# Optimization experiments

Measured on AMD Instinct MI355X. Metric: run time of the kernel, lower is better.

## Reference

```python
import jax, jax.numpy as jnp
import numpy as np

HIDDEN = 2048
INTER = 4096
HEADS = 32
HEAD_DIM = INTER // HEADS  # 128
STATE = 128
GROUPS = 1
CONV_K = 4
CHUNK = 256
EPS = 1e-5
CONV_DIM = INTER + 2 * GROUPS * STATE  # 4352
DT_MIN, DT_MAX = 0.0, 100.0
BATCH, SEQ = 2, 4096


def _segment_sum(x):
    """Stable segment sum: returns (..., T, T) with entry [i,j] = sum_{k=j+1..i} x[k] (-inf above diag)."""
    T = x.shape[-1]
    xx = jnp.broadcast_to(x[..., None], x.shape + (T,))
    mask_lower = jnp.tril(jnp.ones((T, T), bool), -1)
    xx = jnp.where(mask_lower, xx, 0.0)
    seg = jnp.cumsum(xx, axis=-2)
    mask_incl = jnp.tril(jnp.ones((T, T), bool), 0)
    return jnp.where(mask_incl, seg, -jnp.inf)


def setup_inputs() -> dict:
    key = jax.random.key(0)
    ks = jax.random.split(key, 8)
    std = 0.02
    return {
        "hidden_states": jax.random.normal(ks[0], (BATCH, SEQ, HIDDEN), jnp.float32),
        "in_proj_w": jax.random.normal(ks[1], (INTER + CONV_DIM + HEADS, HIDDEN), jnp.float32) * std,
        "conv_w": jax.random.normal(ks[2], (CONV_DIM, 1, CONV_K), jnp.float32) * std,
        "conv_b": jnp.zeros((CONV_DIM,), jnp.float32),
        "A_log": jnp.log(jax.random.uniform(ks[3], (HEADS,), jnp.float32, 1.0, 16.0)),
        "dt_bias": jax.random.normal(ks[4], (HEADS,), jnp.float32) * 0.1,
        "D": jnp.ones((HEADS,), jnp.float32),
        "norm_w": jnp.ones((INTER,), jnp.float32),
        "out_proj_w": jax.random.normal(ks[5], (HIDDEN, INTER), jnp.float32) * (std / np.sqrt(48.0)),
    }


def reference(hidden_states, in_proj_w, conv_w, conv_b, A_log, dt_bias, D, norm_w, out_proj_w):
    b, s, _ = hidden_states.shape
    # in_proj and split into gate / conv-input / dt
    proj = hidden_states @ in_proj_w.T
    gate, hBC, dt = jnp.split(proj, [INTER, INTER + CONV_DIM], axis=-1)

    # causal depthwise conv1d (padding k-1 left, truncate to seq_len) + SiLU
    x = jnp.transpose(hBC, (0, 2, 1))  # (b, conv_dim, s)
    x = jax.lax.conv_general_dilated(
        x, conv_w, window_strides=(1,), padding=[(CONV_K - 1, 0)],
        dimension_numbers=("NCH", "OIH", "NCH"), feature_group_count=CONV_DIM)
    x = x + conv_b[None, :, None]
    hBC = jax.nn.silu(jnp.transpose(x, (0, 2, 1)))  # (b, s, conv_dim)

    xs, B, C = jnp.split(hBC, [INTER, INTER + GROUPS * STATE], axis=-1)

    A = -jnp.exp(A_log)  # (h,)
    dt = jnp.clip(jax.nn.softplus(dt + dt_bias), DT_MIN, DT_MAX)  # (b, s, h)

    xs = xs.reshape(b, s, HEADS, HEAD_DIM)
    rep = HEADS // GROUPS
    Bm = jnp.repeat(B.reshape(b, s, GROUPS, STATE), rep, axis=2)  # (b,s,h,n)
    Cm = jnp.repeat(C.reshape(b, s, GROUPS, STATE), rep, axis=2)

    pad = (-s) % CHUNK

    def padseq(t):
        return jnp.pad(t, ((0, 0), (0, pad)) + ((0, 0),) * (t.ndim - 2))

    D_res = D[None, None, :, None] * padseq(xs)  # (b, S, h, p)
    xdt = padseq(xs * dt[..., None])
    Ad = padseq(A[None, None, :] * dt)  # (b, S, h)
    Bm, Cm = padseq(Bm), padseq(Cm)

    nc = (s + pad) // CHUNK
    xdt = xdt.reshape(b, nc, CHUNK, HEADS, HEAD_DIM)
    Ad = jnp.transpose(Ad.reshape(b, nc, CHUNK, HEADS), (0, 3, 1, 2))  # (b,h,c,l)
    Bm = Bm.reshape(b, nc, CHUNK, HEADS, STATE)
    Cm = Cm.reshape(b, nc, CHUNK, HEADS, STATE)

    A_cum = jnp.cumsum(Ad, axis=-1)  # (b,h,c,l)

    # 1) intra-chunk (diagonal block) output
    L = jnp.exp(_segment_sum(Ad))  # (b,h,c,l,l)
    G = jnp.einsum("bclhn,bcshn->bclsh", Cm, Bm)
    M = G * jnp.transpose(L, (0, 2, 3, 4, 1))
    Y_diag = jnp.einsum("bclsh,bcshp->bclhp", M, xdt)

    # 2) per-chunk final states
    decay_states = jnp.exp(A_cum[:, :, :, -1:] - A_cum)  # (b,h,c,l)
    B_decay = Bm * jnp.transpose(decay_states, (0, 2, 3, 1))[..., None]
    states = jnp.einsum("bclhn,bclhp->bchpn", B_decay, xdt)  # (b,c,h,p,n)

    # 3) inter-chunk recurrence
    states = jnp.concatenate([jnp.zeros_like(states[:, :1]), states], axis=1)  # (b,c+1,h,p,n)
    chunk_sums = jnp.pad(A_cum[:, :, :, -1], ((0, 0), (0, 0), (1, 0)))  # (b,h,c+1)
    decay_chunk = jnp.exp(_segment_sum(chunk_sums))  # (b,h,c+1,c+1)
    decay_chunk = jnp.transpose(decay_chunk, (0, 2, 3, 1))  # (b,c,z,h)
    new_states = jnp.einsum("bczh,bchpn->bzhpn", decay_chunk, states)
    states = new_states[:, :-1]  # (b,c,h,p,n) state entering each chunk

    # 4) state -> output contribution
    state_decay = jnp.exp(A_cum)  # (b,h,c,l)
    Y_off = jnp.einsum("bclhn,bchpn->bclhp", Cm, states) * jnp.transpose(state_decay, (0, 2, 3, 1))[..., None]

    y = (Y_diag + Y_off).reshape(b, nc * CHUNK, HEADS, HEAD_DIM) + D_res
    y = y[:, :s].reshape(b, s, INTER)

    # gated RMSNorm
    y = y * jax.nn.silu(gate)
    var = jnp.mean(y * y, axis=-1, keepdims=True)
    y = y * jax.lax.rsqrt(var + EPS) * norm_w

    return y @ out_proj_w.T
```

## Files before the change

kernel.cpp:

```cpp
#include <hip/hip_runtime.h>

#define SEQ     4096
#define BATCH   2
#define NROWS   8192
#define HID     2048
#define INTER_  4096
#define NHEADS  32
#define HDIM    128
#define NSTATE  128
#define CDIM    4352
#define NPROJ_  8480
#define NPAD    8704
#define NCH     16
#define CHUNK_  256

typedef __attribute__((ext_vector_type(8))) short bf16x8;
typedef __attribute__((ext_vector_type(4))) short short4v;
typedef __attribute__((ext_vector_type(4))) float f32x4;

#define AS1 __attribute__((address_space(1)))
#define AS3 __attribute__((address_space(3)))

__device__ __forceinline__ float bf2f(short s) {
  union { unsigned u; float f; } x;
  x.u = ((unsigned)(unsigned short)s) << 16;
  return x.f;
}
__device__ __forceinline__ short f2bf(float f) {
  union { float f; unsigned u; } x; x.f = f;
  unsigned r = x.u + 0x7FFFu + ((x.u >> 16) & 1u);
  return (short)(r >> 16);
}

__global__ void cvt_bf16(const float* __restrict__ in, short* __restrict__ out,
                         int n4, int nsrc4) {
  int i = blockIdx.x * 256 + threadIdx.x;
  if (i >= n4) return;
  short4v o = {0, 0, 0, 0};
  if (i < nsrc4) {
    f32x4 v = *(const f32x4*)(in + (size_t)i * 4);
    o = (short4v){ f2bf(v.x), f2bf(v.y), f2bf(v.z), f2bf(v.w) };
  }
  *(short4v*)(out + (size_t)i * 4) = o;
}

template<int MODE>
__global__ __launch_bounds__(512, 1)
void gemm256(const short* __restrict__ A, const short* __restrict__ Bw,
             int M, int N, int K, int nM,
             float* __restrict__ outF, short* __restrict__ gate,
             short* __restrict__ hbc, float* __restrict__ dtraw)
{
  __shared__ __align__(16) short lds[2][2][2][256 * 32];
  const int tid = threadIdx.x;
  const int lane = tid & 63, wave = tid >> 6;
  const int l16 = lane & 15, lhi = lane >> 4;
  const int wm = wave >> 2, wn = wave & 3;

  const int bm = blockIdx.x % nM, bn = blockIdx.x / nM;
  const size_t row0 = (size_t)bm * 256;
  const int    col0 = bn * 256;

  const short* Ab  = A + row0 * K;
  const short* Bbp = Bw + (size_t)col0 * K;

  f32x4 acc[8][4];
  #pragma unroll
  for (int m = 0; m < 8; ++m)
    #pragma unroll
    for (int n = 0; n < 4; ++n) acc[m][n] = (f32x4){0.f, 0.f, 0.f, 0.f};

  auto stage = [&](int bufq, int mat, int kh, int ko) {
    const short* gsrc = mat ? Bbp : Ab;
    short* base = &lds[bufq][mat][kh][0];
    #pragma unroll
    for (int j = 0; j < 2; ++j) {
      int u = j * 512 + tid;
      int r = u >> 2;
      int g = (u & 3) ^ ((r >> 1) & 3);
      __builtin_amdgcn_global_load_lds(
          (const AS1 unsigned*)(gsrc + (size_t)r * K + ko + kh * 32 + g * 8),
          (AS3 unsigned*)(base + (j * 512 + wave * 64) * 8), 16, 0, 0);
    }
  };
  auto readA = [&](int bufq, int kh, int mh, bf16x8* a) {
    const short* base = &lds[bufq][0][kh][0];
    #pragma unroll
    for (int f = 0; f < 4; ++f) {
      int rr = wm * 128 + mh * 64 + f * 16 + l16;
      int g = lhi ^ ((rr >> 1) & 3);
      a[f] = *(const bf16x8*)(base + rr * 32 + g * 8);
    }
  };
  auto readB = [&](int bufq, int kh, bf16x8* b) {
    const short* base = &lds[bufq][1][kh][0];
    #pragma unroll
    for (int f = 0; f < 4; ++f) {
      int rr = wn * 64 + f * 16 + l16;
      int g = lhi ^ ((rr >> 1) & 3);
      b[f] = *(const bf16x8*)(base + rr * 32 + g * 8);
    }
  };

  const int nt = K / 64;
  stage(0, 0, 0, 0); stage(0, 1, 0, 0); stage(0, 0, 1, 0); stage(0, 1, 1, 0);
  asm volatile("s_waitcnt vmcnt(4)" ::: "memory");
  __builtin_amdgcn_s_barrier();

  for (int t = 0; t < nt; ++t) {
    const int buf = t & 1, nb = buf ^ 1;
    const int kon = (t + 1) * 64;
    const bool pf = (t + 1 < nt);

    #pragma unroll
    for (int kh = 0; kh < 2; ++kh) {
      if (pf) { stage(nb, 0, kh, kon); stage(nb, 1, kh, kon); }
      bf16x8 a[8], b[4];
      readA(buf, kh, 0, a); readA(buf, kh, 1, a + 4); readB(buf, kh, b);
      __builtin_amdgcn_s_setprio(1);
      #pragma unroll
      for (int mf = 0; mf < 8; ++mf)
        #pragma unroll
        for (int nf = 0; nf < 4; ++nf)
          acc[mf][nf] = __builtin_amdgcn_mfma_f32_16x16x32_bf16(a[mf], b[nf], acc[mf][nf], 0, 0, 0);
      __builtin_amdgcn_s_setprio(0);
      if (pf || kh == 0) {
        if (pf) asm volatile("s_waitcnt vmcnt(4)" ::: "memory");
        else    asm volatile("s_waitcnt vmcnt(0)" ::: "memory");
        __builtin_amdgcn_s_barrier();
      }
    }
  }

  #pragma unroll
  for (int mh = 0; mh < 2; ++mh) {
    #pragma unroll
    for (int f = 0; f < 4; ++f) {
      #pragma unroll
      for (int nf = 0; nf < 4; ++nf) {
        #pragma unroll
        for (int j = 0; j < 4; ++j) {
          int gr = (int)row0 + wm * 128 + mh * 64 + f * 16 + lhi * 4 + j;
          int gc = col0 + wn * 64 + nf * 16 + l16;
          float v = acc[mh * 4 + f][nf][j];
          if (MODE == 0) {
            outF[(size_t)gr * N + gc] = v;
          } else {
            if (gc < INTER_)             gate[(size_t)gr * INTER_ + gc] = f2bf(v);
            else if (gc < INTER_ + CDIM) hbc[(size_t)gr * CDIM + (gc - INTER_)] = f2bf(v);
            else if (gc < NPROJ_)        dtraw[(size_t)gr * NHEADS + (gc - INTER_ - CDIM)] = v;
          }
        }
      }
    }
  }
}

__global__ __launch_bounds__(256)
void conv_t(const short* __restrict__ hbc, const float* __restrict__ cw,
            const float* __restrict__ cb, short* __restrict__ xsT,
            short* __restrict__ Bb, short* __restrict__ Cb, short* __restrict__ BbT)
{
  __shared__ short sOut[64][130];
  int ct = blockIdx.y;
  int cl = threadIdx.x & 127;
  int rh = threadIdx.x >> 7;
  int c = ct * 128 + cl;
  int row0 = blockIdx.x * 64;
  int s0 = row0 & (SEQ - 1);
  float w0 = cw[c * 4 + 0], w1 = cw[c * 4 + 1], w2 = cw[c * 4 + 2], w3 = cw[c * 4 + 3];
  float bias = cb[c];
  int r0 = rh * 32;
  float h0, h1, h2;
  h0 = (s0 + r0 - 3 >= 0) ? bf2f(hbc[(size_t)(row0 + r0 - 3) * CDIM + c]) : 0.f;
  h1 = (s0 + r0 - 2 >= 0) ? bf2f(hbc[(size_t)(row0 + r0 - 2) * CDIM + c]) : 0.f;
  h2 = (s0 + r0 - 1 >= 0) ? bf2f(hbc[(size_t)(row0 + r0 - 1) * CDIM + c]) : 0.f;

  for (int r = r0; r < r0 + 32; ++r) {
    float xin = bf2f(hbc[(size_t)(row0 + r) * CDIM + c]);
    float a = bias + w0 * h0 + w1 * h1 + w2 * h2 + w3 * xin;
    h0 = h1; h1 = h2; h2 = xin;
    float v = a / (1.f + expf(-a));
    short bv = f2bf(v);
    if (ct < 33) sOut[r][cl] = bv;
    if (ct == 32)      Bb[(size_t)(row0 + r) * NSTATE + cl] = bv;
    else if (ct == 33) Cb[(size_t)(row0 + r) * NSTATE + cl] = bv;
  }
  if (ct >= 33) return;
  __syncthreads();
  int p = threadIdx.x >> 1, sh = (threadIdx.x & 1) * 32;
  int b = row0 >> 12;
  size_t dst;
  short* outp;
  if (ct < 32) { outp = xsT; dst = ((size_t)(b * 32 + ct) * 128 + p) * SEQ + s0 + sh; }
  else         { outp = BbT; dst = ((size_t)b * 128 + p) * SEQ + s0 + sh; }
  #pragma unroll
  for (int g = 0; g < 8; ++g) {
    short4v o;
    o[0] = sOut[sh + g * 4 + 0][p];
    o[1] = sOut[sh + g * 4 + 1][p];
    o[2] = sOut[sh + g * 4 + 2][p];
    o[3] = sOut[sh + g * 4 + 3][p];
    *(short4v*)(outp + dst + g * 4) = o;
  }
}

__global__ void dt_proc(const float* __restrict__ dtraw, const float* __restrict__ dtb,
                        float* __restrict__ dtT, int n) {
  int i = blockIdx.x * 256 + threadIdx.x;
  if (i >= n) return;
  float x = dtraw[i] + dtb[i & (NHEADS - 1)];
  float sp = (x > 20.f) ? x : log1pf(expf(x));
  float d = fminf(fmaxf(sp, 0.f), 100.f);
  int row = i >> 5, h = i & 31;
  dtT[(size_t)h * NROWS + row] = d;
}

__global__ __launch_bounds__(256)
void ssm_state(const short* __restrict__ xsT, const short* __restrict__ BbT,
               const float* __restrict__ dtT, const float* __restrict__ Alog,
               short* __restrict__ csb, float* __restrict__ dAsum)
{
  int blk = blockIdx.x;
  int h = blk & 31, cc = (blk >> 5) & 15, b = blk >> 9;
  int tid = threadIdx.x, lane = tid & 63, wave = tid >> 6;
  int l16 = lane & 15, lhi = lane >> 4;
  int s0 = cc * CHUNK_;

  __shared__ float acum[256];
  __shared__ float sdt[256];
  { float Ah = -expf(Alog[h]);
    float d = dtT[(size_t)h * NROWS + (size_t)b * SEQ + s0 + tid];
    sdt[tid] = d; acum[tid] = Ah * d; }
  for (int off = 1; off < 256; off <<= 1) {
    __syncthreads();
    float v = (tid >= off) ? acum[tid - off] : 0.f;
    __syncthreads();
    acum[tid] += v;
  }
  __syncthreads();
  float alast = acum[255];

  const short* xbase = xsT + ((size_t)(b * 32 + h) * 128) * SEQ + s0;
  const short* bbase = BbT + ((size_t)b * 128) * SEQ + s0;

  f32x4 acc[2][8];
  #pragma unroll
  for (int m = 0; m < 2; ++m)
    #pragma unroll
    for (int n = 0; n < 8; ++n) acc[m][n] = (f32x4){0.f, 0.f, 0.f, 0.f};

  for (int lt0 = 0; lt0 < 256; lt0 += 32) {
    float fe[8];
    #pragma unroll
    for (int e = 0; e < 8; ++e) {
      int kl = lt0 + lhi * 8 + e;
      fe[e] = sdt[kl] * __expf(alast - acum[kl]);
    }
    bf16x8 af[2];
    #pragma unroll
    for (int m = 0; m < 2; ++m) {
      bf16x8 raw = *(const bf16x8*)(xbase + (size_t)(wave * 32 + m * 16 + l16) * SEQ + lt0 + lhi * 8);
      bf16x8 sc;
      #pragma unroll
      for (int e = 0; e < 8; ++e) sc[e] = f2bf(bf2f(raw[e]) * fe[e]);
      af[m] = sc;
    }
    #pragma unroll
    for (int n = 0; n < 8; ++n) {
      bf16x8 bfv = *(const bf16x8*)(bbase + (size_t)(n * 16 + l16) * SEQ + lt0 + lhi * 8);
      acc[0][n] = __builtin_amdgcn_mfma_f32_16x16x32_bf16(af[0], bfv, acc[0][n], 0, 0, 0);
      acc[1][n] = __builtin_amdgcn_mfma_f32_16x16x32_bf16(af[1], bfv, acc[1][n], 0, 0, 0);
    }
  }
  size_t base = (size_t)blk * 16384;
  #pragma unroll
  for (int m = 0; m < 2; ++m)
    #pragma unroll
    for (int n = 0; n < 8; ++n)
      #pragma unroll
      for (int j = 0; j < 4; ++j) {
        int p = wave * 32 + m * 16 + lhi * 4 + j;
        int ng = n * 16 + l16;
        csb[base + (size_t)p * NSTATE + ng] = f2bf(acc[m][n][j]);
      }
  if (tid == 0) dAsum[blk] = alast;
}

__global__ void ssm_scan(short* __restrict__ csb, const float* __restrict__ dAsum) {
  int idx = blockIdx.x * 256 + threadIdx.x;
  int np = idx & 16383;
  int bh = idx >> 14;
  int h = bh & 31, b = bh >> 5;
  float run = 0.f;
  #pragma unroll
  for (int c = 0; c < NCH; ++c) {
    size_t base = ((size_t)((b * NCH + c) * NHEADS + h)) * 16384 + np;
    float v = bf2f(csb[base]);
    csb[base] = f2bf(run);
    run = run * __expf(dAsum[(b * NCH + c) * NHEADS + h]) + v;
  }
}

__global__ __launch_bounds__(256)
void ssm_y(const short* __restrict__ xsT, const short* __restrict__ Bb,
           const short* __restrict__ Cb, const float* __restrict__ dtT,
           const float* __restrict__ Alog, const float* __restrict__ Dv,
           const short* __restrict__ csb, short* __restrict__ gateY)
{
  int blk = blockIdx.y, lt = blockIdx.x;
  int h = blk & 31, cc = (blk >> 5) & 15, b = blk >> 9;
  int tid = threadIdx.x, lane = tid & 63, wave = tid >> 6;
  int l16 = lane & 15, lhi = lane >> 4;
  int s0 = cc * CHUNK_;
  size_t row0 = (size_t)b * SEQ + s0;

  __shared__ float acum[256];
  __shared__ float sdt[256];
  __shared__ __align__(16) short M_lds[64 * 264];

  { float Ah = -expf(Alog[h]);
    float d = dtT[(size_t)h * NROWS + row0 + tid];
    sdt[tid] = d; acum[tid] = Ah * d; }
  for (int off = 1; off < 256; off <<= 1) {
    __syncthreads();
    float v = (tid >= off) ? acum[tid - off] : 0.f;
    __syncthreads();
    acum[tid] += v;
  }
  __syncthreads();

  float Dh = Dv[h];

  {
    f32x4 acc1[4][4];
    #pragma unroll
    for (int m = 0; m < 4; ++m)
      #pragma unroll
      for (int n = 0; n < 4; ++n) acc1[m][n] = (f32x4){0.f, 0.f, 0.f, 0.f};
    for (int kk = 0; kk < NSTATE; kk += 32) {
      bf16x8 af[4], bv[4];
      #pragma unroll
      for (int m = 0; m < 4; ++m)
        af[m] = *(const bf16x8*)(Cb + (row0 + lt * 64 + m * 16 + l16) * NSTATE + kk + lhi * 8);
      #pragma unroll
      for (int n = 0; n < 4; ++n)
        bv[n] = *(const bf16x8*)(Bb + (row0 + wave * 64 + n * 16 + l16) * NSTATE + kk + lhi * 8);
      #pragma unroll
      for (int m = 0; m < 4; ++m)
        #pragma unroll
        for (int n = 0; n < 4; ++n)
          acc1[m][n] = __builtin_amdgcn_mfma_f32_16x16x32_bf16(af[m], bv[n], acc1[m][n], 0, 0, 0);
    }
    float as_[4]; int sg_[4];
    #pragma unroll
    for (int n = 0; n < 4; ++n) { sg_[n] = wave * 64 + n * 16 + l16; as_[n] = acum[sg_[n]]; }
    #pragma unroll
    for (int m = 0; m < 4; ++m) {
      #pragma unroll
      for (int j = 0; j < 4; ++j) {
        int ll = m * 16 + lhi * 4 + j;
        int lg = lt * 64 + ll;
        float al = acum[lg];
        float dinv = Dh / fmaxf(sdt[lg], 1e-20f);
        #pragma unroll
        for (int n = 0; n < 4; ++n) {
          float v = 0.f;
          if (sg_[n] <= lg) {
            v = acc1[m][n][j] * __expf(al - as_[n]);
            if (sg_[n] == lg) v += dinv;
          }
          M_lds[ll * 264 + wave * 64 + n * 16 + l16] = f2bf(v);
        }
      }
    }
  }
  __syncthreads();

  const short* xbase = xsT + ((size_t)(b * 32 + h) * 128) * SEQ + s0;

  f32x4 accY[4][2];
  #pragma unroll
  for (int m = 0; m < 4; ++m) { accY[m][0] = (f32x4){0,0,0,0}; accY[m][1] = (f32x4){0,0,0,0}; }
  int smax = (lt + 1) * 64;
  for (int st = 0; st < smax; st += 32) {
    float fe[8];
    #pragma unroll
    for (int e = 0; e < 8; ++e) fe[e] = sdt[st + lhi * 8 + e];
    bf16x8 bv2[2];
    #pragma unroll
    for (int n = 0; n < 2; ++n) {
      bf16x8 raw = *(const bf16x8*)(xbase + (size_t)(wave * 32 + n * 16 + l16) * SEQ + st + lhi * 8);
      bf16x8 sc;
      #pragma unroll
      for (int e = 0; e < 8; ++e) sc[e] = f2bf(bf2f(raw[e]) * fe[e]);
      bv2[n] = sc;
    }
    #pragma unroll
    for (int m = 0; m < 4; ++m) {
      bf16x8 a = *(const bf16x8*)(M_lds + (m * 16 + l16) * 264 + st + lhi * 8);
      accY[m][0] = __builtin_amdgcn_mfma_f32_16x16x32_bf16(a, bv2[0], accY[m][0], 0, 0, 0);
      accY[m][1] = __builtin_amdgcn_mfma_f32_16x16x32_bf16(a, bv2[1], accY[m][1], 0, 0, 0);
    }
  }

  f32x4 accO[4][2];
  #pragma unroll
  for (int m = 0; m < 4; ++m) { accO[m][0] = (f32x4){0,0,0,0}; accO[m][1] = (f32x4){0,0,0,0}; }
  const short* sbase = csb + (size_t)blk * 16384;
  for (int nt = 0; nt < NSTATE; nt += 32) {
    bf16x8 bv2[2];
    #pragma unroll
    for (int n = 0; n < 2; ++n) {
      int p = wave * 32 + n * 16 + l16;
      bv2[n] = *(const bf16x8*)(sbase + (size_t)p * NSTATE + nt + lhi * 8);
    }
    #pragma unroll
    for (int m = 0; m < 4; ++m) {
      bf16x8 a = *(const bf16x8*)(Cb + (row0 + lt * 64 + m * 16 + l16) * NSTATE + nt + lhi * 8);
      accO[m][0] = __builtin_amdgcn_mfma_f32_16x16x32_bf16(a, bv2[0], accO[m][0], 0, 0, 0);
      accO[m][1] = __builtin_amdgcn_mfma_f32_16x16x32_bf16(a, bv2[1], accO[m][1], 0, 0, 0);
    }
  }

  #pragma unroll
  for (int m = 0; m < 4; ++m) {
    #pragma unroll
    for (int j = 0; j < 4; ++j) {
      int ll = m * 16 + lhi * 4 + j;
      float e = __expf(acum[lt * 64 + ll]);
      size_t row = row0 + lt * 64 + ll;
      #pragma unroll
      for (int n = 0; n < 2; ++n) {
        int p = wave * 32 + n * 16 + l16;
        size_t adr = row * INTER_ + h * HDIM + p;
        float yv = accY[m][n][j] + e * accO[m][n][j];
        float g = bf2f(gateY[adr]);
        gateY[adr] = f2bf(yv * g / (1.f + expf(-g)));
      }
    }
  }
}

__global__ __launch_bounds__(256)
void gate_norm(short* __restrict__ ybf, const float* __restrict__ nw)
{
  int row = blockIdx.x;
  int tid = threadIdx.x;
  size_t base = (size_t)row * INTER_;
  float vals[16];
  float ss = 0.f;
  #pragma unroll
  for (int i = 0; i < 16; ++i) {
    int idx = tid + i * 256;
    float v = bf2f(ybf[base + idx]);
    vals[i] = v;
    ss += v * v;
  }
  #pragma unroll
  for (int off = 32; off > 0; off >>= 1) ss += __shfl_down(ss, off);
  __shared__ float ws4[4];
  if ((tid & 63) == 0) ws4[tid >> 6] = ss;
  __syncthreads();
  float tot = ws4[0] + ws4[1] + ws4[2] + ws4[3];
  float scale = rsqrtf(tot * (1.f / 4096.f) + 1e-5f);
  #pragma unroll
  for (int i = 0; i < 16; ++i) {
    int idx = tid + i * 256;
    ybf[base + idx] = f2bf(vals[i] * scale * nw[idx]);
  }
}

extern "C" void kernel_launch(void* const* d_in, const int* in_sizes, int n_in,
                              void* d_out, int out_size, void* d_ws, size_t ws_size,
                              hipStream_t stream)
{
  const float* Xf   = (const float*)d_in[0];
  const float* W1f  = (const float*)d_in[1];
  const float* cw   = (const float*)d_in[2];
  const float* cb   = (const float*)d_in[3];
  const float* Alog = (const float*)d_in[4];
  const float* dtb  = (const float*)d_in[5];
  const float* Dv   = (const float*)d_in[6];
  const float* nw   = (const float*)d_in[7];
  const float* W2f  = (const float*)d_in[8];
  float* outp = (float*)d_out;
  char* ws = (char*)d_ws;

  size_t off = 0;
  short* Xb  = (short*)(ws + off); off += (size_t)NROWS * HID * 2;
  short* W1b = (short*)(ws + off); off += (size_t)NPAD * HID * 2;
  short* xsT = (short*)ws;
  short* W2b = (short*)(ws + off); off += (size_t)HID * INTER_ * 2;
  short* gateY = (short*)(ws + off); off += (size_t)NROWS * INTER_ * 2;
  short* hbc  = (short*)(ws + off); off += (size_t)NROWS * CDIM * 2;
  float* dtv  = (float*)(ws + off); off += (size_t)NROWS * NHEADS * 4;
  float* dtT  = (float*)(ws + off); off += (size_t)NROWS * NHEADS * 4;
  short* Bb   = (short*)(ws + off); off += (size_t)NROWS * NSTATE * 2;
  short* Cb   = (short*)(ws + off); off += (size_t)NROWS * NSTATE * 2;
  short* BbT  = (short*)(ws + off); off += (size_t)NROWS * NSTATE * 2;
  float* dAs  = (float*)(ws + off); off += 4096;
  short* csb  = (short*)hbc;

  cvt_bf16<<<(NROWS * HID / 4 + 255) / 256, 256, 0, stream>>>(
      Xf, Xb, NROWS * HID / 4, NROWS * HID / 4);
  cvt_bf16<<<(NPAD * HID / 4 + 255) / 256, 256, 0, stream>>>(
      W1f, W1b, NPAD * HID / 4, NPROJ_ * HID / 4);
  cvt_bf16<<<(HID * INTER_ / 4 + 255) / 256, 256, 0, stream>>>(
      W2f, W2b, HID * INTER_ / 4, HID * INTER_ / 4);

  gemm256<1><<<(NROWS / 256) * (NPAD / 256), 512, 0, stream>>>(
      Xb, W1b, NROWS, NPROJ_, HID, NROWS / 256, nullptr, gateY, hbc, dtv);

  dt_proc<<<(NROWS * NHEADS) / 256, 256, 0, stream>>>(dtv, dtb, dtT, NROWS * NHEADS);
  conv_t<<<dim3(NROWS / 64, 34), 256, 0, stream>>>(hbc, cw, cb, xsT, Bb, Cb, BbT);

  ssm_state<<<BATCH * NCH * NHEADS, 256, 0, stream>>>(xsT, BbT, dtT, Alog, csb, dAs);
  ssm_scan<<<(BATCH * NHEADS * 16384) / 256, 256, 0, stream>>>(csb, dAs);
  ssm_y<<<dim3(4, BATCH * NCH * NHEADS), 256, 0, stream>>>(xsT, Bb, Cb, dtT, Alog, Dv, csb, gateY);

  gate_norm<<<NROWS, 256, 0, stream>>>(gateY, nw);

  gemm256<0><<<(NROWS / 256) * (HID / 256), 512, 0, stream>>>(
      gateY, W2b, NROWS, HID, INTER_, NROWS / 256, outp, nullptr, nullptr, nullptr);
}
```

Measured before the change: 842.6 us.

## Split GEMM k-step into four interleaved read/stage/MFMA phases with barriers

Restructures the GEMM main loop into four phases per tile, each issuing a small set of LDS fragment reads and one global->LDS stage, then a barrier and a 16-MFMA quad. It also halves the A-fragment registers held at once, from eight to four. The aim is to interleave memory traffic with MFMA work in a ping-pong style and lower register pressure. In exchange it adds extra workgroup barriers and lgkmcnt waits per k-tile, which could serialize the waves.

Result: no change. 855.1 us (+1.5%).

```diff
diff --git a/kernel.cpp b/kernel.cpp
--- a/kernel.cpp
+++ b/kernel.cpp
@@ -102,6 +102,18 @@
     }
   };
 
+  bf16x8 bfr[4];
+  auto quad = [&](int mh, const bf16x8* a) {
+    __builtin_amdgcn_s_setprio(1);
+    #pragma unroll
+    for (int f = 0; f < 4; ++f)
+      #pragma unroll
+      for (int nf = 0; nf < 4; ++nf)
+        acc[mh * 4 + f][nf] =
+            __builtin_amdgcn_mfma_f32_16x16x32_bf16(a[f], bfr[nf], acc[mh * 4 + f][nf], 0, 0, 0);
+    __builtin_amdgcn_s_setprio(0);
+  };
+
   const int nt = K / 64;
   stage(0, 0, 0, 0); stage(0, 1, 0, 0); stage(0, 0, 1, 0); stage(0, 1, 1, 0);
   asm volatile("s_waitcnt vmcnt(4)" ::: "memory");
@@ -111,25 +123,38 @@
     const int buf = t & 1, nb = buf ^ 1;
     const int kon = (t + 1) * 64;
     const bool pf = (t + 1 < nt);
-
-    #pragma unroll
-    for (int kh = 0; kh < 2; ++kh) {
-      if (pf) { stage(nb, 0, kh, kon); stage(nb, 1, kh, kon); }
-      bf16x8 a[8], b[4];
-      readA(buf, kh, 0, a); readA(buf, kh, 1, a + 4); readB(buf, kh, b);
-      __builtin_amdgcn_s_setprio(1);
-      #pragma unroll
-      for (int mf = 0; mf < 8; ++mf)
-        #pragma unroll
-        for (int nf = 0; nf < 4; ++nf)
-          acc[mf][nf] = __builtin_amdgcn_mfma_f32_16x16x32_bf16(a[mf], b[nf], acc[mf][nf], 0, 0, 0);
-      __builtin_amdgcn_s_setprio(0);
-      if (pf || kh == 0) {
-        if (pf) asm volatile("s_waitcnt vmcnt(4)" ::: "memory");
-        else    asm volatile("s_waitcnt vmcnt(0)" ::: "memory");
-        __builtin_amdgcn_s_barrier();
-      }
-    }
+    bf16x8 a[4];
+
+    readB(buf, 0, bfr); readA(buf, 0, 0, a);
+    if (pf) stage(nb, 0, 0, kon);
+    __builtin_amdgcn_s_barrier();
+    asm volatile("s_waitcnt lgkmcnt(0)" ::: "memory");
+    quad(0, a);
+    __builtin_amdgcn_s_barrier();
+
+    readA(buf, 0, 1, a);
+    if (pf) stage(nb, 1, 0, kon);
+    __builtin_amdgcn_s_barrier();
+    asm volatile("s_waitcnt lgkmcnt(0)" ::: "memory");
+    quad(1, a);
+    if (pf) asm volatile("s_waitcnt vmcnt(4)" ::: "memory");
+    else    asm volatile("s_waitcnt vmcnt(0)" ::: "memory");
+    __builtin_amdgcn_s_barrier();
+
+    readB(buf, 1, bfr); readA(buf, 1, 0, a);
+    if (pf) stage(nb, 0, 1, kon);
+    __builtin_amdgcn_s_barrier();
+    asm volatile("s_waitcnt lgkmcnt(0)" ::: "memory");
+    quad(0, a);
+    __builtin_amdgcn_s_barrier();
+
+    readA(buf, 1, 1, a);
+    if (pf) stage(nb, 1, 1, kon);
+    __builtin_amdgcn_s_barrier();
+    asm volatile("s_waitcnt lgkmcnt(0)" ::: "memory");
+    quad(1, a);
+    if (pf) asm volatile("s_waitcnt vmcnt(4)" ::: "memory");
+    __builtin_amdgcn_s_barrier();
   }
 
   #pragma unroll
```
